# Optimization experiments

Measured on AMD Instinct MI355X. Metric: run time of the kernel, lower is better.

## Reference

```python
import jax, jax.numpy as jnp
import numpy as np

T, B, D = 256, 64, 512


def setup_inputs() -> dict:
    key = jax.random.key(0)
    ks = jax.random.split(key, 9)
    s = 1.0 / np.sqrt(D)  # torch Linear default init scale (uniform), use scaled normal
    return {
        "x": jax.random.normal(ks[0], (T, B, D), dtype=jnp.float32),
        "y": jax.random.normal(ks[1], (T, B, D), dtype=jnp.float32),
        "Wr": jax.random.normal(ks[2], (D, D), dtype=jnp.float32) * s,
        "Ur": jax.random.normal(ks[3], (D, D), dtype=jnp.float32) * s,
        "Wz": jax.random.normal(ks[4], (D, D), dtype=jnp.float32) * s,
        "Uz": jax.random.normal(ks[5], (D, D), dtype=jnp.float32) * s,
        "Wg": jax.random.normal(ks[6], (D, D), dtype=jnp.float32) * s,
        "Ug": jax.random.normal(ks[7], (D, D), dtype=jnp.float32) * s,
        "bg": jnp.full((D,), 2.0, dtype=jnp.float32),
    }


def reference(x, y, Wr, Ur, Wz, Uz, Wg, Ug, bg):
    # GTrXL gating unit. torch Linear(y) == y @ W.T
    r = jax.nn.sigmoid(jnp.einsum("tbd,ed->tbe", y, Wr) + jnp.einsum("tbd,ed->tbe", x, Ur))
    z = jax.nn.sigmoid(jnp.einsum("tbd,ed->tbe", y, Wz) + jnp.einsum("tbd,ed->tbe", x, Uz) - bg)
    h = jnp.tanh(jnp.einsum("tbd,ed->tbe", y, Wg) + jnp.einsum("tbd,ed->tbe", r * x, Ug))
    g = (1.0 - z) * x + z * h  # (T, B, D)
    return g
```

## Files before the change

### kernel.cpp

```cpp
#include <hip/hip_runtime.h>
#include <stdint.h>

typedef unsigned short u16;
typedef __attribute__((ext_vector_type(8))) __bf16 bf16x8;
typedef __attribute__((ext_vector_type(4))) float f32x4;

#define Dn 512
#define Mn 16384


__device__ __forceinline__ u16 f2bf(float f) {
  unsigned u = __float_as_uint(f);
  u += 0x7fffu + ((u >> 16) & 1u);
  return (u16)(u >> 16);
}

__device__ __forceinline__ float bf2f(u16 b) {
  return __uint_as_float(((unsigned)b) << 16);
}

__device__ __forceinline__ void async16(const u16* g, u16* l) {
  __builtin_amdgcn_global_load_lds(
      (const __attribute__((address_space(1))) unsigned int*)g,
      (__attribute__((address_space(3))) unsigned int*)l, 16, 0, 0);
}

__device__ __forceinline__ float sigmoidf_(float v) {
  return 1.f / (1.f + __expf(-v));
}

__global__ void cast_all(const float* __restrict__ y, const float* __restrict__ x,
                         const float* w0, const float* w1, const float* w2,
                         const float* w3, const float* w4, const float* w5,
                         u16* __restrict__ yb, u16* __restrict__ xb,
                         u16* __restrict__ bRZ, u16* __restrict__ bG) {
  int b = blockIdx.x;
  const int t = (int)threadIdx.x;
  if (b < 16384) {
    const float* src;
    u16* dst;
    if (b < 8192) { src = y; dst = yb; }
    else          { src = x; dst = xb; b -= 8192; }
    const int i4 = b * 256 + t;
    float4 v = ((const float4*)src)[i4];
    ushort4 o;
    o.x = f2bf(v.x); o.y = f2bf(v.y); o.z = f2bf(v.z); o.w = f2bf(v.w);
    ((ushort4*)dst)[i4] = o;
    return;
  }
  b -= 16384;
  const int wi = b >> 8;
  const int bb = b & 255;
  const float* src = wi == 0 ? w0 : wi == 1 ? w1 : wi == 2 ? w2
                   : wi == 3 ? w3 : wi == 4 ? w4 : w5;
  const int i4 = bb * 256 + t;
  const int e  = i4 >> 7;
  const int c4 = i4 & 127;
  float4 v = ((const float4*)src)[i4];
  ushort4 o;
  o.x = f2bf(v.x); o.y = f2bf(v.y); o.z = f2bf(v.z); o.w = f2bf(v.w);
  ushort4* base = (wi >= 4) ? (ushort4*)bG : (ushort4*)bRZ;
  const int row = e + ((wi == 2 || wi == 3) ? 512 : 0);
  const int off = row * 256 + c4 + ((wi & 1) ? 128 : 0);
  base[off] = o;
}

__global__ __launch_bounds__(256, 4) void gemm_rz1(
    const u16* __restrict__ yb, const u16* __restrict__ xb,
    const u16* __restrict__ bRZ, const float* __restrict__ bg,
    u16* __restrict__ rxb, u16* __restrict__ zb) {
  __shared__ u16 smem[16384];
  u16* sA = smem;
  u16* sB = smem + 8192;

  const int tid = threadIdx.x;
  const int lane = tid & 63;
  const int wave = tid >> 6;
  const int waveM = wave >> 1, waveN = wave & 1;
  const int mb = blockIdx.x & 127, nb = blockIdx.x >> 7;
  const int rowStart = mb * 128, colStart = nb * 128;
  const int wbyte = (tid & 192) * 16;
  const int lm = lane & 15, quad = lane >> 4;

  const int srow = tid >> 3;
  const int scol = (((tid & 7) ^ ((tid >> 3) & 7)) * 8);
  const int lswz = lm & 7;

  f32x4 acc[4][4] = {};

  for (int kq = 0; kq < 16; ++kq) {
    const int half = kq >> 3;
    const int k0 = (kq & 7) * 64;
    const u16* abase = half ? xb : yb;
#pragma unroll
    for (int s = 0; s < 4; ++s) {
      async16(abase + (size_t)(rowStart + s * 32 + srow) * 512 + k0 + scol,
              (u16*)((char*)sA + s * 4096 + wbyte));
      async16(bRZ + (size_t)(colStart + s * 32 + srow) * 1024 + kq * 64 + scol,
              (u16*)((char*)sB + s * 4096 + wbyte));
    }
    __syncthreads();

#pragma unroll
    for (int kk = 0; kk < 2; ++kk) {
      bf16x8 aa[4], bw[4];
#pragma unroll
      for (int i = 0; i < 4; ++i)
        aa[i] = *(const bf16x8*)(sA + (waveM * 64 + i * 16 + lm) * 64 +
                                 ((kk * 4 + quad) ^ lswz) * 8);
#pragma unroll
      for (int j = 0; j < 4; ++j)
        bw[j] = *(const bf16x8*)(sB + (waveN * 64 + j * 16 + lm) * 64 +
                                 ((kk * 4 + quad) ^ lswz) * 8);
#pragma unroll
      for (int i = 0; i < 4; ++i)
#pragma unroll
        for (int j = 0; j < 4; ++j)
          acc[i][j] = __builtin_amdgcn_mfma_f32_16x16x32_bf16(aa[i], bw[j], acc[i][j], 0, 0, 0);
    }
    __syncthreads();
  }

  if (colStart < 512) {
#pragma unroll
    for (int j = 0; j < 4; ++j) {
      const int e = colStart + waveN * 64 + j * 16 + lm;
#pragma unroll
      for (int i = 0; i < 4; ++i) {
        const int m0 = rowStart + waveM * 64 + i * 16 + quad * 4;
#pragma unroll
        for (int rg = 0; rg < 4; ++rg) {
          const size_t idx = (size_t)(m0 + rg) * 512 + e;
          const float r = sigmoidf_(acc[i][j][rg]);
          rxb[idx] = f2bf(r * bf2f(xb[idx]));
        }
      }
    }
  } else {
#pragma unroll
    for (int j = 0; j < 4; ++j) {
      const int e = colStart - 512 + waveN * 64 + j * 16 + lm;
      const float bgv = bg[e];
#pragma unroll
      for (int i = 0; i < 4; ++i) {
        const int m0 = rowStart + waveM * 64 + i * 16 + quad * 4;
#pragma unroll
        for (int rg = 0; rg < 4; ++rg) {
          const size_t idx = (size_t)(m0 + rg) * 512 + e;
          zb[idx] = f2bf(sigmoidf_(acc[i][j][rg] - bgv));
        }
      }
    }
  }
}

__global__ __launch_bounds__(256, 4) void gemm_gu1(
    const u16* __restrict__ yb, const u16* __restrict__ rxb,
    const u16* __restrict__ bG,
    const u16* __restrict__ zb, const u16* __restrict__ xb,
    float* __restrict__ out) {
  __shared__ u16 smem[16384];
  u16* sA = smem;
  u16* sB = smem + 8192;

  const int tid = threadIdx.x;
  const int lane = tid & 63;
  const int wave = tid >> 6;
  const int waveM = wave >> 1, waveN = wave & 1;
  const int mb = blockIdx.x & 127, nb = blockIdx.x >> 7;
  const int rowStart = mb * 128, colStart = nb * 128;
  const int wbyte = (tid & 192) * 16;
  const int lm = lane & 15, quad = lane >> 4;

  const int srow = tid >> 3;
  const int scol = (((tid & 7) ^ ((tid >> 3) & 7)) * 8);
  const int lswz = lm & 7;

  f32x4 acc[4][4] = {};

  for (int kq = 0; kq < 16; ++kq) {
    const int half = kq >> 3;
    const int k0 = (kq & 7) * 64;
    const u16* abase = half ? rxb : yb;
#pragma unroll
    for (int s = 0; s < 4; ++s) {
      async16(abase + (size_t)(rowStart + s * 32 + srow) * 512 + k0 + scol,
              (u16*)((char*)sA + s * 4096 + wbyte));
      async16(bG + (size_t)(colStart + s * 32 + srow) * 1024 + kq * 64 + scol,
              (u16*)((char*)sB + s * 4096 + wbyte));
    }
    __syncthreads();

#pragma unroll
    for (int kk = 0; kk < 2; ++kk) {
      bf16x8 aa[4], bw[4];
#pragma unroll
      for (int i = 0; i < 4; ++i)
        aa[i] = *(const bf16x8*)(sA + (waveM * 64 + i * 16 + lm) * 64 +
                                 ((kk * 4 + quad) ^ lswz) * 8);
#pragma unroll
      for (int j = 0; j < 4; ++j)
        bw[j] = *(const bf16x8*)(sB + (waveN * 64 + j * 16 + lm) * 64 +
                                 ((kk * 4 + quad) ^ lswz) * 8);
#pragma unroll
      for (int i = 0; i < 4; ++i)
#pragma unroll
        for (int j = 0; j < 4; ++j)
          acc[i][j] = __builtin_amdgcn_mfma_f32_16x16x32_bf16(aa[i], bw[j], acc[i][j], 0, 0, 0);
    }
    __syncthreads();
  }

#pragma unroll
  for (int j = 0; j < 4; ++j) {
    const int e = colStart + waveN * 64 + j * 16 + lm;
#pragma unroll
    for (int i = 0; i < 4; ++i) {
      const int m0 = rowStart + waveM * 64 + i * 16 + quad * 4;
#pragma unroll
      for (int rg = 0; rg < 4; ++rg) {
        const size_t idx = (size_t)(m0 + rg) * 512 + e;
        const float pre = acc[i][j][rg];
        const float ex = __expf(-2.f * pre);
        const float h = (1.f - ex) / (1.f + ex);
        const float z = bf2f(zb[idx]);
        const float xv = bf2f(xb[idx]);
        out[idx] = (1.f - z) * xv + z * h;
      }
    }
  }
}

extern "C" void kernel_launch(void* const* d_in, const int* in_sizes, int n_in,
                              void* d_out, int out_size, void* d_ws, size_t ws_size,
                              hipStream_t stream) {
  const float* x  = (const float*)d_in[0];
  const float* y  = (const float*)d_in[1];
  const float* Wr = (const float*)d_in[2];
  const float* Ur = (const float*)d_in[3];
  const float* Wz = (const float*)d_in[4];
  const float* Uz = (const float*)d_in[5];
  const float* Wg = (const float*)d_in[6];
  const float* Ug = (const float*)d_in[7];
  const float* bg = (const float*)d_in[8];
  float* out = (float*)d_out;

  char* ws = (char*)d_ws;
  u16* yb  = (u16*)(ws);
  u16* xb  = (u16*)(ws + 16777216);
  u16* rxb = (u16*)(ws + 2 * 16777216);
  u16* zb  = (u16*)(ws + 3 * 16777216);
  u16* bRZ = (u16*)(ws + 4 * 16777216);
  u16* bG  = (u16*)(ws + 4 * 16777216 + 2097152);

  cast_all<<<17920, 256, 0, stream>>>(y, x, Wr, Ur, Wz, Uz, Wg, Ug, yb, xb, bRZ, bG);
  gemm_rz1<<<1024, 256, 0, stream>>>(yb, xb, bRZ, bg, rxb, zb);
  gemm_gu1<<<512, 256, 0, stream>>>(yb, rxb, bG, zb, xb, out);
}
```

Measured before the change: 199.8 us.

## Rewrite RZ GEMM with 256x256 tiles and 4-stage async LDS pipeline

The r/z GEMM moves from 128x128 tiles with 256 threads and a single LDS buffer to 256x256 tiles with 512 threads. It adds a 4-deep ring of async global-to-LDS stages using a K step of 32, manual vmcnt waits, barriers and MFMA priority boosting. Loads for later stages are meant to overlap MFMA work, and the larger tile cuts global traffic per FLOP. In exchange the kernel uses 128KB of LDS and 128 accumulator registers per thread, and launches only 256 blocks, which risks low occupancy and an uneven tail across the CUs.

Result: slower. 212.5 us (+6.4%).

```diff
diff --git a/kernel.cpp b/kernel.cpp
--- a/kernel.cpp
+++ b/kernel.cpp
@@ -65,60 +65,72 @@
   base[off] = o;
 }
 
-__global__ __launch_bounds__(256, 4) void gemm_rz1(
+__global__ __launch_bounds__(512, 2) void gemm_rz2(
     const u16* __restrict__ yb, const u16* __restrict__ xb,
     const u16* __restrict__ bRZ, const float* __restrict__ bg,
     u16* __restrict__ rxb, u16* __restrict__ zb) {
-  __shared__ u16 smem[16384];
-  u16* sA = smem;
-  u16* sB = smem + 8192;
+  __shared__ u16 smem[65536];
 
   const int tid = threadIdx.x;
   const int lane = tid & 63;
   const int wave = tid >> 6;
-  const int waveM = wave >> 1, waveN = wave & 1;
-  const int mb = blockIdx.x & 127, nb = blockIdx.x >> 7;
-  const int rowStart = mb * 128, colStart = nb * 128;
-  const int wbyte = (tid & 192) * 16;
+  const int waveM = wave >> 2;
+  const int waveN = wave & 3;
+  const int mb = blockIdx.x & 63, nb = blockIdx.x >> 6;
+  const int rowStart = mb * 256, colStart = nb * 256;
   const int lm = lane & 15, quad = lane >> 4;
-
-  const int srow = tid >> 3;
-  const int scol = (((tid & 7) ^ ((tid >> 3) & 7)) * 8);
-  const int lswz = lm & 7;
-
-  f32x4 acc[4][4] = {};
-
-  for (int kq = 0; kq < 16; ++kq) {
-    const int half = kq >> 3;
-    const int k0 = (kq & 7) * 64;
-    const u16* abase = half ? xb : yb;
-#pragma unroll
-    for (int s = 0; s < 4; ++s) {
-      async16(abase + (size_t)(rowStart + s * 32 + srow) * 512 + k0 + scol,
-              (u16*)((char*)sA + s * 4096 + wbyte));
-      async16(bRZ + (size_t)(colStart + s * 32 + srow) * 1024 + kq * 64 + scol,
-              (u16*)((char*)sB + s * 4096 + wbyte));
-    }
-    __syncthreads();
-
-#pragma unroll
-    for (int kk = 0; kk < 2; ++kk) {
-      bf16x8 aa[4], bw[4];
-#pragma unroll
-      for (int i = 0; i < 4; ++i)
-        aa[i] = *(const bf16x8*)(sA + (waveM * 64 + i * 16 + lm) * 64 +
-                                 ((kk * 4 + quad) ^ lswz) * 8);
+  const int aoff = (quad ^ ((lm >> 1) & 3)) * 8;
+
+  const int srow = tid >> 2;
+  const int lc = ((tid & 3) ^ ((srow >> 1) & 3)) * 8;
+  const int woff = wave * 1024;
+
+  f32x4 acc[8][4] = {};
+
+  auto STAGE = [&](int t) {
+    const u16* abase = (t < 16) ? yb : xb;
+    const int k0 = (t & 15) * 32;
+    char* s = (char*)(smem + ((t & 3) << 14));
+    async16(abase + (size_t)(rowStart + srow) * 512 + k0 + lc, (u16*)(s + woff));
+    async16(abase + (size_t)(rowStart + 128 + srow) * 512 + k0 + lc, (u16*)(s + 8192 + woff));
+    async16(bRZ + (size_t)(colStart + srow) * 1024 + t * 32 + lc, (u16*)(s + 16384 + woff));
+    async16(bRZ + (size_t)(colStart + 128 + srow) * 1024 + t * 32 + lc, (u16*)(s + 24576 + woff));
+  };
+
+  STAGE(0); STAGE(1); STAGE(2); STAGE(3);
+  __builtin_amdgcn_sched_barrier(0);
+
+  for (int t = 0; t < 32; ++t) {
+    if (t < 29)       asm volatile("s_waitcnt vmcnt(12)" ::: "memory");
+    else if (t == 29) asm volatile("s_waitcnt vmcnt(8)" ::: "memory");
+    else if (t == 30) asm volatile("s_waitcnt vmcnt(4)" ::: "memory");
+    else              asm volatile("s_waitcnt vmcnt(0)" ::: "memory");
+    __builtin_amdgcn_sched_barrier(0);
+    __builtin_amdgcn_s_barrier();
+
+    const u16* sA = smem + ((t & 3) << 14);
+    const u16* sB = sA + 8192;
+    bf16x8 aa[8], bw[4];
+#pragma unroll
+    for (int i = 0; i < 8; ++i)
+      aa[i] = *(const bf16x8*)(sA + (waveM * 128 + i * 16 + lm) * 32 + aoff);
+#pragma unroll
+    for (int j = 0; j < 4; ++j)
+      bw[j] = *(const bf16x8*)(sB + (waveN * 64 + j * 16 + lm) * 32 + aoff);
+    asm volatile("s_waitcnt lgkmcnt(0)" ::: "memory");
+    __builtin_amdgcn_sched_barrier(0);
+    __builtin_amdgcn_s_barrier();
+
+    if (t < 28) STAGE(t + 4);
+    __builtin_amdgcn_sched_barrier(0);
+
+    __builtin_amdgcn_s_setprio(1);
+#pragma unroll
+    for (int i = 0; i < 8; ++i)
 #pragma unroll
       for (int j = 0; j < 4; ++j)
-        bw[j] = *(const bf16x8*)(sB + (waveN * 64 + j * 16 + lm) * 64 +
-                                 ((kk * 4 + quad) ^ lswz) * 8);
-#pragma unroll
-      for (int i = 0; i < 4; ++i)
-#pragma unroll
-        for (int j = 0; j < 4; ++j)
-          acc[i][j] = __builtin_amdgcn_mfma_f32_16x16x32_bf16(aa[i], bw[j], acc[i][j], 0, 0, 0);
-    }
-    __syncthreads();
+        acc[i][j] = __builtin_amdgcn_mfma_f32_16x16x32_bf16(aa[i], bw[j], acc[i][j], 0, 0, 0);
+    __builtin_amdgcn_s_setprio(0);
   }
 
   if (colStart < 512) {
@@ -126,8 +138,8 @@
     for (int j = 0; j < 4; ++j) {
       const int e = colStart + waveN * 64 + j * 16 + lm;
 #pragma unroll
-      for (int i = 0; i < 4; ++i) {
-        const int m0 = rowStart + waveM * 64 + i * 16 + quad * 4;
+      for (int i = 0; i < 8; ++i) {
+        const int m0 = rowStart + waveM * 128 + i * 16 + quad * 4;
 #pragma unroll
         for (int rg = 0; rg < 4; ++rg) {
           const size_t idx = (size_t)(m0 + rg) * 512 + e;
@@ -142,8 +154,8 @@
       const int e = colStart - 512 + waveN * 64 + j * 16 + lm;
       const float bgv = bg[e];
 #pragma unroll
-      for (int i = 0; i < 4; ++i) {
-        const int m0 = rowStart + waveM * 64 + i * 16 + quad * 4;
+      for (int i = 0; i < 8; ++i) {
+        const int m0 = rowStart + waveM * 128 + i * 16 + quad * 4;
 #pragma unroll
         for (int rg = 0; rg < 4; ++rg) {
           const size_t idx = (size_t)(m0 + rg) * 512 + e;
@@ -254,6 +266,6 @@
   u16* bG  = (u16*)(ws + 4 * 16777216 + 2097152);
 
   cast_all<<<17920, 256, 0, stream>>>(y, x, Wr, Ur, Wz, Uz, Wg, Ug, yb, xb, bRZ, bG);
-  gemm_rz1<<<1024, 256, 0, stream>>>(yb, xb, bRZ, bg, rxb, zb);
+  gemm_rz2<<<256, 512, 0, stream>>>(yb, xb, bRZ, bg, rxb, zb);
   gemm_gu1<<<512, 256, 0, stream>>>(yb, rxb, bG, zb, xb, out);
 }
```
